# Optimization experiments

Measured on AMD Instinct MI355X. Metric: run time of the kernel, lower is better.

Reference implementation:

```python
import jax, jax.numpy as jnp
import numpy as np

B, N, F_IN, F_HID, F_EMB, H, L_DIM = 8, 1024, 128, 128, 128, 8, 2


def _xavier(key, shape, fan_in, fan_out):
    lim = np.sqrt(6.0 / (fan_in + fan_out))
    return jax.random.uniform(key, shape, jnp.float32, -lim, lim)


def setup_inputs() -> dict:
    key = jax.random.key(0)
    ks = jax.random.split(key, 16)
    x = jax.random.normal(ks[0], (B, N, F_IN), jnp.float32)
    # sparse 0/1 adjacency with self loops (avoids fully-masked softmax rows)
    adj = (jax.random.uniform(ks[1], (B, N, N)) < 0.05).astype(jnp.float32)
    adj = jnp.maximum(adj, jnp.eye(N, dtype=jnp.float32)[None])
    def gat_params(k, f_in, f_out):
        k1, k2, k3 = jax.random.split(k, 3)
        return (_xavier(k1, (H, f_in, f_out), f_in, f_out),
                _xavier(k2, (H, f_out, 1), f_out, 1),
                _xavier(k3, (H, f_out, 1), f_out, 1),
                jnp.zeros((f_out,), jnp.float32))
    w1, as1, ad1, b1 = gat_params(ks[2], F_IN, F_HID)
    w2, as2, ad2, b2 = gat_params(ks[3], F_HID, F_HID)
    w3, as3, ad3, b3 = gat_params(ks[4], F_HID, F_EMB)
    pred_in = F_HID * 2 + F_EMB  # hidden*(num_layers-1)+embedding, concat=True
    pw = _xavier(ks[5], (pred_in, L_DIM), pred_in, L_DIM)
    pb = jnp.zeros((L_DIM,), jnp.float32)
    return {"x": x, "adj": adj,
            "w1": w1, "as1": as1, "ad1": ad1, "b1": b1,
            "w2": w2, "as2": as2, "ad2": ad2, "b2": b2,
            "w3": w3, "as3": as3, "ad3": ad3, "b3": b3,
            "pw": pw, "pb": pb}


def gat_layer(h, adj, w, a_src, a_dst, bias):
    # h: [B,N,f_in] -> h_prime: [B,H,N,f_out]
    hp = jnp.einsum('bnf,hfo->bhno', h, w)
    t = jnp.tanh(hp)
    s = jnp.einsum('bhno,hoi->bhni', t, a_src)[..., 0]  # [B,H,N]
    d = jnp.einsum('bhno,hoi->bhni', t, a_dst)[..., 0]  # [B,H,N]
    scores = s[:, :, :, None] + d[:, :, None, :]        # [B,H,N,N]
    scores = jnp.where(scores >= 0, scores, 0.2 * scores)  # LeakyReLU(0.2)
    scores = jnp.where(adj[:, None, :, :] > 0, scores, -jnp.inf)
    attn = jax.nn.softmax(scores, axis=-1)  # dropout disabled (eval mode)
    out = jnp.einsum('bhnm,bhmo->bhno', attn, hp) + bias
    return out.mean(axis=1)  # merge heads -> [B,N,f_out]


def reference(x, adj, w1, as1, ad1, b1, w2, as2, ad2, b2, w3, as3, ad3, b3, pw, pb):
    x1 = jax.nn.relu(gat_layer(x, adj, w1, as1, ad1, b1))
    x2 = jax.nn.relu(gat_layer(x1, adj, w2, as2, ad2, b2))
    x3 = gat_layer(x2, adj, w3, as3, ad3, b3)
    x_all = jnp.concatenate([x1, x2, x3], axis=2)  # [B,N,pred_in]
    pooled = jnp.max(x_all, axis=1)                # max over nodes -> [B,pred_in]
    return pooled @ pw + pb                        # [B,label_dim]
```

## Files before the change

### kernel.cpp

```cpp
#include <hip/hip_runtime.h>
#include <hip/hip_fp16.h>

#define BB 8
#define NN 1024
#define FF 128
#define HH 8

typedef _Float16 f16;
typedef f16  f16x8 __attribute__((ext_vector_type(8)));
typedef f16  f16x4 __attribute__((ext_vector_type(4)));
typedef float f32x4 __attribute__((ext_vector_type(4)));

#define L2E 1.44269504f

__device__ __forceinline__ float lrelu(float x){ return fmaxf(x, 0.2f*x); }


__global__ void k_conv_x(const float* __restrict__ x, f16* __restrict__ o){
  int i = (blockIdx.x*256 + threadIdx.x)*8;
  float4 a = *(const float4*)(x+i), b = *(const float4*)(x+i+4);
  f16x8 v;
  v[0]=(f16)a.x; v[1]=(f16)a.y; v[2]=(f16)a.z; v[3]=(f16)a.w;
  v[4]=(f16)b.x; v[5]=(f16)b.y; v[6]=(f16)b.z; v[7]=(f16)b.w;
  *(f16x8*)(o+i) = v;
}

__global__ void k_conv_w(const float* __restrict__ w1, const float* __restrict__ w2,
                         const float* __restrict__ w3, f16* __restrict__ wB){
  int e = blockIdx.x*256 + threadIdx.x;
  int fc = e & 15, c = (e>>4)&127, h = (e>>11)&7, l = e>>14;
  const float* w = (l==0) ? w1 : ((l==1) ? w2 : w3);
  f16x8 v;
  #pragma unroll
  for(int j=0;j<8;j++) v[j] = (f16)w[(h*128 + fc*8 + j)*128 + c];
  *(f16x8*)(wB + (((l*8+h)*16 + fc)*128 + c)*8) = v;
}

__global__ void k_adjm(const float* __restrict__ adj, unsigned* __restrict__ am){
  int wv = threadIdx.x >> 6, lane = threadIdx.x & 63;
  int r = blockIdx.x*4 + wv;
  const float* row = adj + (long)r*1024;
  for(int g=0; g<16; g++){
    float v = row[g*64 + lane];
    unsigned long long mb = __ballot(v > 0.0f);
    if (lane == 0){
      am[r*32 + 2*g]   = (unsigned)mb;
      am[r*32 + 2*g+1] = (unsigned)(mb >> 32);
    }
  }
}

__global__ __launch_bounds__(256,2) void k_hp(
    const f16* __restrict__ xin,
    const f16* __restrict__ wBl,
    const float* __restrict__ asrc, const float* __restrict__ adst,
    f16* __restrict__ hpB,
    float* __restrict__ sarr, float* __restrict__ darr)
{
  __shared__ f16 xs[128*136];
  __shared__ float asl[128], adl[128];
  int t = threadIdx.x;
  int bid = blockIdx.x;
  int it = bid & 7, h = (bid>>3)&7, b = bid>>6;
  int i0 = it*128;
  {
    const f16* src = xin + (long)(b*1024 + i0)*128;
    int fc = t & 15, r0 = t >> 4;
    #pragma unroll
    for(int p=0;p<8;p++){
      int r = r0 + p*16;
      f16x8 v = *(const f16x8*)(src + r*128 + fc*8);
      *(f16x8*)(xs + r*136 + fc*8) = v;
    }
  }
  if (t < 128){ asl[t] = asrc[h*128+t]; adl[t] = adst[h*128+t]; }
  __syncthreads();

  int lane = t & 63, wv = t>>6, wr = wv>>1, wc = wv&1;
  int mq = lane & 15, quad = lane >> 4;
  f32x4 acc[4][4];
  #pragma unroll
  for(int a=0;a<4;a++)
    #pragma unroll
    for(int c=0;c<4;c++) acc[a][c] = (f32x4){0.f,0.f,0.f,0.f};

  const f16* wh = wBl + h*16*128*8;
  #pragma unroll
  for(int ks=0; ks<4; ks++){
    f16x8 af[4], bf[4];
    #pragma unroll
    for(int mt=0; mt<4; mt++)
      af[mt] = *(const f16x8*)(xs + (wr*64 + mt*16 + mq)*136 + ks*32 + quad*8);
    #pragma unroll
    for(int nt=0; nt<4; nt++){
      int c  = wc*64 + nt*16 + mq;
      int fc = ks*4 + quad;
      bf[nt] = *(const f16x8*)(wh + (fc*128 + c)*8);
    }
    #pragma unroll
    for(int mt=0; mt<4; mt++)
      #pragma unroll
      for(int nt=0; nt<4; nt++)
        acc[mt][nt] = __builtin_amdgcn_mfma_f32_16x16x32_f16(af[mt], bf[nt], acc[mt][nt], 0,0,0);
  }
  __syncthreads();
  f16* tt = xs;
  f16* hpb = hpB + (long)(b*8+h)*128*128*8;
  #pragma unroll
  for(int mt=0; mt<4; mt++){
    #pragma unroll
    for(int nt=0; nt<4; nt++){
      int c = wc*64 + nt*16 + mq;
      f16x4 pk;
      #pragma unroll
      for(int rg=0; rg<4; rg++){
        float v = acc[mt][nt][rg];
        pk[rg] = (f16)v;
        int il = wr*64 + mt*16 + quad*4 + rg;
        float e2 = __expf(2.0f*v);
        float th = 1.0f - 2.0f*__builtin_amdgcn_rcpf(e2 + 1.0f);
        tt[il*136 + c] = (f16)th;
      }
      int il0 = wr*64 + mt*16 + quad*4;
      int inode = i0 + il0;
      *(f16x4*)(hpb + ((long)(inode>>3)*128 + c)*8 + (inode&7)) = pk;
    }
  }
  __syncthreads();
  {
    int r = t>>1, hf = t&1;
    float s_p = 0.f, d_p = 0.f;
    #pragma unroll
    for(int q=0;q<8;q++){
      f16x8 tv = *(const f16x8*)(tt + r*136 + hf*64 + q*8);
      #pragma unroll
      for(int j=0;j<8;j++){
        float tvf = (float)tv[j];
        int c = hf*64 + q*8 + j;
        s_p = fmaf(tvf, asl[c], s_p);
        d_p = fmaf(tvf, adl[c], d_p);
      }
    }
    s_p += __shfl_xor(s_p, 1);
    d_p += __shfl_xor(d_p, 1);
    if (hf == 0){
      sarr[(b*8+h)*1024 + i0 + r] = s_p;
      darr[(b*8+h)*1024 + i0 + r] = d_p;
    }
  }
}

__global__ __launch_bounds__(256,4) void k_attn(
    const f16* __restrict__ hpB,
    const float* __restrict__ sarr, const float* __restrict__ darr,
    const unsigned* __restrict__ am,
    f16* __restrict__ part,
    float* __restrict__ zpart)
{
  __shared__ float ddl[512];
  __shared__ float wred[4];
  __shared__ f16 Pl[2][128*40];
  int t = threadIdx.x;
  int bid = blockIdx.x;
  int bh = bid & 63, q = bid >> 6;
  int jh = q & 1, it = q >> 1;
  int i0 = it*128, j0 = jh*512;
  int b = bh >> 3;

  {
    float4 v = *(const float4*)(darr + bh*1024 + t*4);
    float mx = fmaxf(fmaxf(v.x,v.y), fmaxf(v.z,v.w));
    #pragma unroll
    for(int o=1;o<64;o<<=1) mx = fmaxf(mx, __shfl_xor(mx, o));
    if ((t&63)==0) wred[t>>6] = mx;
    int base = t*4 - j0;
    if (base >= 0 && base < 512){
      float4 s = make_float4(v.x*L2E, v.y*L2E, v.z*L2E, v.w*L2E);
      *(float4*)(ddl + base) = s;
    }
  }
  __syncthreads();
  float Dml = fmaxf(fmaxf(wred[0],wred[1]), fmaxf(wred[2],wred[3])) * L2E;

  int prow = t>>1, pjg = t&1;
  float srowl = sarr[bh*1024 + i0 + prow] * L2E;
  float ml = srowl + Dml;
  float mrowl = fmaxf(ml, 0.2f*ml);
  const unsigned* amrow = am + ((long)(b*1024 + i0 + prow))*32 + jh*16;

  int lane = t&63, wv = t>>6, wr = wv>>1, wc = wv&1;
  int mq = lane&15, quad = lane>>4;
  const f16* hpb = hpB + (long)bh*128*128*8;
  f32x4 acc[4][4];
  #pragma unroll
  for(int a=0;a<4;a++)
    #pragma unroll
    for(int c=0;c<4;c++) acc[a][c] = (f32x4){0.f,0.f,0.f,0.f};
  float zacc = 0.f;
  f16x8 zerov = (f16x8){0,0,0,0,0,0,0,0};

  unsigned wcur = amrow[0];
  for(int jt=0; jt<16; jt++){
    f16x8 bf[4];
    #pragma unroll
    for(int nt=0;nt<4;nt++){
      int c  = wc*64 + nt*16 + mq;
      int jc = jh*64 + jt*4 + quad;
      bf[nt] = *(const f16x8*)(hpb + (jc*128 + c)*8);
    }
    unsigned wnx = (jt < 15) ? amrow[jt+1] : 0u;
    f16* Pb = Pl[jt&1];
    f16* myp = Pb + prow*40 + pjg*16;
    *(f16x8*)(myp)     = zerov;
    *(f16x8*)(myp + 8) = zerov;
    unsigned word = (wcur >> (pjg*16)) & 0xffffu;
    const float* dloc = ddl + jt*32 + pjg*16;
    while(word){
      int j = __builtin_ctz(word);
      word &= word - 1u;
      float xl  = srowl + dloc[j];
      float scl = fmaxf(xl, 0.2f*xl);
      float e   = __builtin_amdgcn_exp2f(scl - mrowl);
      zacc += e;
      myp[j] = (f16)e;
    }
    __syncthreads();
    #pragma unroll
    for(int mt=0;mt<4;mt++){
      f16x8 a = *(const f16x8*)(Pb + (wr*64 + mt*16 + mq)*40 + quad*8);
      #pragma unroll
      for(int nt=0;nt<4;nt++)
        acc[mt][nt] = __builtin_amdgcn_mfma_f32_16x16x32_f16(a, bf[nt], acc[mt][nt], 0,0,0);
    }
    wcur = wnx;
  }
  zacc += __shfl_xor(zacc, 1);
  if (pjg == 0) zpart[(jh*64 + bh)*1024 + i0 + prow] = zacc;
  f16* pout = part + ((long)(jh*64 + bh)*1024 + i0)*128;
  #pragma unroll
  for(int mt=0;mt<4;mt++){
    #pragma unroll
    for(int nt=0;nt<4;nt++){
      int c = wc*64 + nt*16 + mq;
      #pragma unroll
      for(int rg=0;rg<4;rg++){
        int il = wr*64 + mt*16 + quad*4 + rg;
        pout[il*128 + c] = (f16)acc[mt][nt][rg];
      }
    }
  }
}

__global__ void k_zinv(const float* __restrict__ zp, float* __restrict__ zinv){
  int i = blockIdx.x*256 + threadIdx.x;
  zinv[i] = 0.125f / (zp[i] + zp[65536 + i]);
}

__global__ void k_fin(const f16* __restrict__ part, const float* __restrict__ zinv,
                      const float* __restrict__ bias,
                      float* __restrict__ x32, f16* __restrict__ x16, int do_relu){
  int idx = blockIdx.x*256 + threadIdx.x;
  int c8 = idx & 15, n = (idx>>4)&1023, b = idx>>14;
  float s[8];
  #pragma unroll
  for(int j=0;j<8;j++) s[j] = 0.f;
  #pragma unroll
  for(int h=0;h<8;h++){
    int bh = b*8 + h;
    float zi = zinv[bh*1024 + n];
    f16x8 p0 = *(const f16x8*)(part + ((long)bh*1024 + n)*128 + c8*8);
    f16x8 p1 = *(const f16x8*)(part + ((long)(64+bh)*1024 + n)*128 + c8*8);
    #pragma unroll
    for(int j=0;j<8;j++) s[j] = fmaf((float)p0[j] + (float)p1[j], zi, s[j]);
  }
  int o = (b*1024 + n)*128 + c8*8;
  f16x8 h8;
  float ov[8];
  #pragma unroll
  for(int j=0;j<8;j++){
    float v = s[j] + bias[c8*8 + j];
    if (do_relu) v = fmaxf(v, 0.f);
    ov[j] = v;
    h8[j] = (f16)v;
  }
  *(float4*)(x32 + o)     = make_float4(ov[0],ov[1],ov[2],ov[3]);
  *(float4*)(x32 + o + 4) = make_float4(ov[4],ov[5],ov[6],ov[7]);
  if (x16) *(f16x8*)(x16 + o) = h8;
}

__global__ void k_pool1(const float* __restrict__ x1, const float* __restrict__ x2,
                        const float* __restrict__ x3, float* __restrict__ pP){
  int bid = blockIdx.x;
  int ch = bid & 7, b = bid >> 3;
  int t = threadIdx.x;
  for(int f = t; f < 384; f += 256){
    const float* buf = (f < 128) ? x1 : ((f < 256) ? x2 : x3);
    int c = f & 127;
    const float* p = buf + ((long)b*1024 + ch*128)*128 + c;
    float mx = -3.4e38f;
    for(int n=0;n<128;n++) mx = fmaxf(mx, p[n*128]);
    pP[bid*384 + f] = mx;
  }
}

__global__ void k_pool2(const float* __restrict__ pP, const float* __restrict__ pw,
                        const float* __restrict__ pb, float* __restrict__ out){
  __shared__ float pl[384];
  int b = blockIdx.x, t = threadIdx.x;
  for(int f = t; f < 384; f += 256){
    float mx = -3.4e38f;
    #pragma unroll
    for(int ch=0;ch<8;ch++) mx = fmaxf(mx, pP[(b*8+ch)*384 + f]);
    pl[f] = mx;
  }
  __syncthreads();
  if (t < 64){
    float a0 = 0.f, a1 = 0.f;
    #pragma unroll
    for(int k=0;k<6;k++){
      int f = t + 64*k;
      float v = pl[f];
      a0 = fmaf(v, pw[f*2],   a0);
      a1 = fmaf(v, pw[f*2+1], a1);
    }
    #pragma unroll
    for(int o=1;o<64;o<<=1){ a0 += __shfl_xor(a0,o); a1 += __shfl_xor(a1,o); }
    if (t == 0){ out[b*2] = a0 + pb[0]; out[b*2+1] = a1 + pb[1]; }
  }
}

extern "C" void kernel_launch(void* const* d_in, const int* in_sizes, int n_in,
                              void* d_out, int out_size, void* d_ws, size_t ws_size,
                              hipStream_t stream) {
  const float* x   = (const float*)d_in[0];
  const float* adj = (const float*)d_in[1];
  const float* w1  = (const float*)d_in[2];
  const float* as1 = (const float*)d_in[3];
  const float* ad1 = (const float*)d_in[4];
  const float* b1  = (const float*)d_in[5];
  const float* w2  = (const float*)d_in[6];
  const float* as2 = (const float*)d_in[7];
  const float* ad2 = (const float*)d_in[8];
  const float* b2  = (const float*)d_in[9];
  const float* w3  = (const float*)d_in[10];
  const float* as3 = (const float*)d_in[11];
  const float* ad3 = (const float*)d_in[12];
  const float* b3  = (const float*)d_in[13];
  const float* pw  = (const float*)d_in[14];
  const float* pb  = (const float*)d_in[15];

  char* ws = (char*)d_ws;
  f16*      x16a = (f16*)ws;                 ws += (size_t)1048576*2;
  f16*      x16b = (f16*)ws;                 ws += (size_t)1048576*2;
  f16*      wB   = (f16*)ws;                 ws += (size_t)393216*2;
  unsigned* am   = (unsigned*)ws;            ws += (size_t)8*1024*32*4;
  f16*      hpB  = (f16*)ws;                 ws += (size_t)8*8*1024*128*2;
  float*    sarr = (float*)ws;               ws += (size_t)65536*4;
  float*    darr = (float*)ws;               ws += (size_t)65536*4;
  f16*      part = (f16*)ws;                 ws += (size_t)2*64*1024*128*2;
  float*    zp   = (float*)ws;               ws += (size_t)2*65536*4;
  float*    zinv = (float*)ws;               ws += (size_t)65536*4;
  float*    x32_1= (float*)ws;               ws += (size_t)1048576*4;
  float*    x32_2= (float*)ws;               ws += (size_t)1048576*4;
  float*    x32_3= (float*)ws;               ws += (size_t)1048576*4;
  float*    pP   = (float*)ws;               ws += (size_t)8*8*384*4;

  k_conv_x<<<512, 256, 0, stream>>>(x, x16a);
  k_conv_w<<<192, 256, 0, stream>>>(w1, w2, w3, wB);
  k_adjm<<<2048, 256, 0, stream>>>(adj, am);

  k_hp  <<<512, 256, 0, stream>>>(x16a, wB,            as1, ad1, hpB, sarr, darr);
  k_attn<<<1024,256, 0, stream>>>(hpB, sarr, darr, am, part, zp);
  k_zinv<<<256, 256, 0, stream>>>(zp, zinv);
  k_fin <<<512, 256, 0, stream>>>(part, zinv, b1, x32_1, x16b, 1);
  k_hp  <<<512, 256, 0, stream>>>(x16b, wB + 131072,   as2, ad2, hpB, sarr, darr);
  k_attn<<<1024,256, 0, stream>>>(hpB, sarr, darr, am, part, zp);
  k_zinv<<<256, 256, 0, stream>>>(zp, zinv);
  k_fin <<<512, 256, 0, stream>>>(part, zinv, b2, x32_2, x16a, 1);
  k_hp  <<<512, 256, 0, stream>>>(x16a, wB + 262144,   as3, ad3, hpB, sarr, darr);
  k_attn<<<1024,256, 0, stream>>>(hpB, sarr, darr, am, part, zp);
  k_zinv<<<256, 256, 0, stream>>>(zp, zinv);
  k_fin <<<512, 256, 0, stream>>>(part, zinv, b3, x32_3, nullptr, 0);

  k_pool1<<<64, 256, 0, stream>>>(x32_1, x32_2, x32_3, pP);
  k_pool2<<<8,  256, 0, stream>>>(pP, pw, pb, (float*)d_out);
}
```

Before: 292.9 us.

## Fuse preprocessing kernels, fold zinv and pooling into finalize, raise occupancy bounds

Merges the three input-conversion kernels into one launch and computes the softmax normalizer inline in k_fin instead of in a separate kernel. k_fin now writes per-block partial column maxima rather than full fp32 layer outputs, so pool1 and the three fp32 activation buffers disappear. Launch bounds for k_hp and k_attn are raised to request higher occupancy, which may cost registers or cause spills. Together these cut launch count and global memory traffic.

```diff
diff --git a/kernel.cpp b/kernel.cpp
--- a/kernel.cpp
+++ b/kernel.cpp
@@ -13,44 +13,42 @@
 
 #define L2E 1.44269504f
 
-__device__ __forceinline__ float lrelu(float x){ return fmaxf(x, 0.2f*x); }
-
-
-__global__ void k_conv_x(const float* __restrict__ x, f16* __restrict__ o){
-  int i = (blockIdx.x*256 + threadIdx.x)*8;
-  float4 a = *(const float4*)(x+i), b = *(const float4*)(x+i+4);
-  f16x8 v;
-  v[0]=(f16)a.x; v[1]=(f16)a.y; v[2]=(f16)a.z; v[3]=(f16)a.w;
-  v[4]=(f16)b.x; v[5]=(f16)b.y; v[6]=(f16)b.z; v[7]=(f16)b.w;
-  *(f16x8*)(o+i) = v;
-}
-
-__global__ void k_conv_w(const float* __restrict__ w1, const float* __restrict__ w2,
-                         const float* __restrict__ w3, f16* __restrict__ wB){
-  int e = blockIdx.x*256 + threadIdx.x;
-  int fc = e & 15, c = (e>>4)&127, h = (e>>11)&7, l = e>>14;
-  const float* w = (l==0) ? w1 : ((l==1) ? w2 : w3);
-  f16x8 v;
-  #pragma unroll
-  for(int j=0;j<8;j++) v[j] = (f16)w[(h*128 + fc*8 + j)*128 + c];
-  *(f16x8*)(wB + (((l*8+h)*16 + fc)*128 + c)*8) = v;
-}
-
-__global__ void k_adjm(const float* __restrict__ adj, unsigned* __restrict__ am){
-  int wv = threadIdx.x >> 6, lane = threadIdx.x & 63;
-  int r = blockIdx.x*4 + wv;
-  const float* row = adj + (long)r*1024;
-  for(int g=0; g<16; g++){
-    float v = row[g*64 + lane];
-    unsigned long long mb = __ballot(v > 0.0f);
-    if (lane == 0){
-      am[r*32 + 2*g]   = (unsigned)mb;
-      am[r*32 + 2*g+1] = (unsigned)(mb >> 32);
-    }
-  }
-}
-
-__global__ __launch_bounds__(256,2) void k_hp(
+__global__ void k_pre(const float* __restrict__ x, f16* __restrict__ x16a,
+                      const float* __restrict__ w1, const float* __restrict__ w2,
+                      const float* __restrict__ w3, f16* __restrict__ wB,
+                      const float* __restrict__ adj, unsigned* __restrict__ am){
+  int bid = blockIdx.x, t = threadIdx.x;
+  if (bid < 512){
+    int i = (bid*256 + t)*8;
+    float4 a = *(const float4*)(x+i), b = *(const float4*)(x+i+4);
+    f16x8 v;
+    v[0]=(f16)a.x; v[1]=(f16)a.y; v[2]=(f16)a.z; v[3]=(f16)a.w;
+    v[4]=(f16)b.x; v[5]=(f16)b.y; v[6]=(f16)b.z; v[7]=(f16)b.w;
+    *(f16x8*)(x16a+i) = v;
+  } else if (bid < 704){
+    int e = (bid-512)*256 + t;
+    int fc = e & 15, c = (e>>4)&127, h = (e>>11)&7, l = e>>14;
+    const float* w = (l==0) ? w1 : ((l==1) ? w2 : w3);
+    f16x8 v;
+    #pragma unroll
+    for(int j=0;j<8;j++) v[j] = (f16)w[(h*128 + fc*8 + j)*128 + c];
+    *(f16x8*)(wB + (((l*8+h)*16 + fc)*128 + c)*8) = v;
+  } else {
+    int wv = t >> 6, lane = t & 63;
+    int r = (bid-704)*4 + wv;
+    const float* row = adj + (long)r*1024;
+    for(int g=0; g<16; g++){
+      float v = row[g*64 + lane];
+      unsigned long long mb = __ballot(v > 0.0f);
+      if (lane == 0){
+        am[r*32 + 2*g]   = (unsigned)mb;
+        am[r*32 + 2*g+1] = (unsigned)(mb >> 32);
+      }
+    }
+  }
+}
+
+__global__ __launch_bounds__(256,3) void k_hp(
     const f16* __restrict__ xin,
     const f16* __restrict__ wBl,
     const float* __restrict__ asrc, const float* __restrict__ adst,
@@ -150,7 +148,7 @@
   }
 }
 
-__global__ __launch_bounds__(256,4) void k_attn(
+__global__ __launch_bounds__(256,6) void k_attn(
     const f16* __restrict__ hpB,
     const float* __restrict__ sarr, const float* __restrict__ darr,
     const unsigned* __restrict__ am,
@@ -251,15 +249,12 @@
   }
 }
 
-__global__ void k_zinv(const float* __restrict__ zp, float* __restrict__ zinv){
-  int i = blockIdx.x*256 + threadIdx.x;
-  zinv[i] = 0.125f / (zp[i] + zp[65536 + i]);
-}
-
-__global__ void k_fin(const f16* __restrict__ part, const float* __restrict__ zinv,
+__global__ void k_fin(const f16* __restrict__ part, const float* __restrict__ zp,
                       const float* __restrict__ bias,
-                      float* __restrict__ x32, f16* __restrict__ x16, int do_relu){
-  int idx = blockIdx.x*256 + threadIdx.x;
+                      f16* __restrict__ x16, float* __restrict__ pmax, int do_relu){
+  __shared__ float pm[16][128];
+  int t = threadIdx.x;
+  int idx = blockIdx.x*256 + t;
   int c8 = idx & 15, n = (idx>>4)&1023, b = idx>>14;
   float s[8];
   #pragma unroll
@@ -267,13 +262,12 @@
   #pragma unroll
   for(int h=0;h<8;h++){
     int bh = b*8 + h;
-    float zi = zinv[bh*1024 + n];
+    float zi = 0.125f / (zp[bh*1024 + n] + zp[65536 + bh*1024 + n]);
     f16x8 p0 = *(const f16x8*)(part + ((long)bh*1024 + n)*128 + c8*8);
     f16x8 p1 = *(const f16x8*)(part + ((long)(64+bh)*1024 + n)*128 + c8*8);
     #pragma unroll
     for(int j=0;j<8;j++) s[j] = fmaf((float)p0[j] + (float)p1[j], zi, s[j]);
   }
-  int o = (b*1024 + n)*128 + c8*8;
   f16x8 h8;
   float ov[8];
   #pragma unroll
@@ -283,34 +277,28 @@
     ov[j] = v;
     h8[j] = (f16)v;
   }
-  *(float4*)(x32 + o)     = make_float4(ov[0],ov[1],ov[2],ov[3]);
-  *(float4*)(x32 + o + 4) = make_float4(ov[4],ov[5],ov[6],ov[7]);
-  if (x16) *(f16x8*)(x16 + o) = h8;
-}
-
-__global__ void k_pool1(const float* __restrict__ x1, const float* __restrict__ x2,
-                        const float* __restrict__ x3, float* __restrict__ pP){
-  int bid = blockIdx.x;
-  int ch = bid & 7, b = bid >> 3;
-  int t = threadIdx.x;
-  for(int f = t; f < 384; f += 256){
-    const float* buf = (f < 128) ? x1 : ((f < 256) ? x2 : x3);
-    int c = f & 127;
-    const float* p = buf + ((long)b*1024 + ch*128)*128 + c;
-    float mx = -3.4e38f;
-    for(int n=0;n<128;n++) mx = fmaxf(mx, p[n*128]);
-    pP[bid*384 + f] = mx;
-  }
-}
-
-__global__ void k_pool2(const float* __restrict__ pP, const float* __restrict__ pw,
+  if (x16) *(f16x8*)(x16 + ((long)(b*1024+n))*128 + c8*8) = h8;
+  #pragma unroll
+  for(int j=0;j<8;j++) pm[n&15][c8*8+j] = ov[j];
+  __syncthreads();
+  if (t < 128){
+    float m = pm[0][t];
+    #pragma unroll
+    for(int r=1;r<16;r++) m = fmaxf(m, pm[r][t]);
+    pmax[blockIdx.x*128 + t] = m;
+  }
+}
+
+__global__ void k_pool2(const float* __restrict__ pmax, const float* __restrict__ pw,
                         const float* __restrict__ pb, float* __restrict__ out){
   __shared__ float pl[384];
   int b = blockIdx.x, t = threadIdx.x;
   for(int f = t; f < 384; f += 256){
+    int l = f >> 7, c = f & 127;
+    const float* p = pmax + l*65536 + b*64*128 + c;
     float mx = -3.4e38f;
-    #pragma unroll
-    for(int ch=0;ch<8;ch++) mx = fmaxf(mx, pP[(b*8+ch)*384 + f]);
+    #pragma unroll 8
+    for(int k=0;k<64;k++) mx = fmaxf(mx, p[k*128]);
     pl[f] = mx;
   }
   __syncthreads();
@@ -359,29 +347,19 @@
   float*    darr = (float*)ws;               ws += (size_t)65536*4;
   f16*      part = (f16*)ws;                 ws += (size_t)2*64*1024*128*2;
   float*    zp   = (float*)ws;               ws += (size_t)2*65536*4;
-  float*    zinv = (float*)ws;               ws += (size_t)65536*4;
-  float*    x32_1= (float*)ws;               ws += (size_t)1048576*4;
-  float*    x32_2= (float*)ws;               ws += (size_t)1048576*4;
-  float*    x32_3= (float*)ws;               ws += (size_t)1048576*4;
-  float*    pP   = (float*)ws;               ws += (size_t)8*8*384*4;
-
-  k_conv_x<<<512, 256, 0, stream>>>(x, x16a);
-  k_conv_w<<<192, 256, 0, stream>>>(w1, w2, w3, wB);
-  k_adjm<<<2048, 256, 0, stream>>>(adj, am);
+  float*    pmax = (float*)ws;               ws += (size_t)3*512*128*4;
+
+  k_pre<<<2752, 256, 0, stream>>>(x, x16a, w1, w2, w3, wB, adj, am);
 
   k_hp  <<<512, 256, 0, stream>>>(x16a, wB,            as1, ad1, hpB, sarr, darr);
   k_attn<<<1024,256, 0, stream>>>(hpB, sarr, darr, am, part, zp);
-  k_zinv<<<256, 256, 0, stream>>>(zp, zinv);
-  k_fin <<<512, 256, 0, stream>>>(part, zinv, b1, x32_1, x16b, 1);
+  k_fin <<<512, 256, 0, stream>>>(part, zp, b1, x16b, pmax,           1);
   k_hp  <<<512, 256, 0, stream>>>(x16b, wB + 131072,   as2, ad2, hpB, sarr, darr);
   k_attn<<<1024,256, 0, stream>>>(hpB, sarr, darr, am, part, zp);
-  k_zinv<<<256, 256, 0, stream>>>(zp, zinv);
-  k_fin <<<512, 256, 0, stream>>>(part, zinv, b2, x32_2, x16a, 1);
+  k_fin <<<512, 256, 0, stream>>>(part, zp, b2, x16a, pmax + 65536,   1);
   k_hp  <<<512, 256, 0, stream>>>(x16a, wB + 262144,   as3, ad3, hpB, sarr, darr);
   k_attn<<<1024,256, 0, stream>>>(hpB, sarr, darr, am, part, zp);
-  k_zinv<<<256, 256, 0, stream>>>(zp, zinv);
-  k_fin <<<512, 256, 0, stream>>>(part, zinv, b3, x32_3, nullptr, 0);
-
-  k_pool1<<<64, 256, 0, stream>>>(x32_1, x32_2, x32_3, pP);
-  k_pool2<<<8,  256, 0, stream>>>(pP, pw, pb, (float*)d_out);
-}
+  k_fin <<<512, 256, 0, stream>>>(part, zp, b3, nullptr, pmax + 131072, 0);
+
+  k_pool2<<<8, 256, 0, stream>>>(pmax, pw, pb, (float*)d_out);
+}
```

After: 485.5 us. 65.8% more time.
